# Performance work log

Hardware: AMD Instinct MI355X
Metric: run time of the kernel (lower is better)

## Reference

```python
import jax, jax.numpy as jnp
import numpy as np

D = 1024      # model_dim
H = 2048      # expert hidden_dim
E = 8         # num routed experts
S = 1         # num shared experts
M = 4         # num modes (1 shared expert per mode)
TOP_K = 2
B, L = 2, 2048


def _ffn(x, w1, b1, w2, b2):
    # x: [T, D]; w1: [..., D, H]; stacked experts via einsum
    h = jnp.einsum('td,edh->teh', x, w1) + b1          # [T, E*, H]
    h = jax.nn.gelu(h)
    return jnp.einsum('teh,ehd->ted', h, w2) + b2      # [T, E*, D]


def setup_inputs() -> dict:
    key = jax.random.key(0)
    ks = jax.random.split(key, 16)
    s = 0.02
    inp = {
        'hidden': jax.random.normal(ks[0], (B, L, D), dtype=jnp.float32),
        'mode_ids': jax.random.randint(ks[1], (B, L), 0, M),
        'router_w': jax.random.normal(ks[2], (D, E), dtype=jnp.float32) * s,
        'router_b': jnp.zeros((E,), dtype=jnp.float32),
        'shared_w1': jax.random.normal(ks[3], (S, D, H), dtype=jnp.float32) * s,
        'shared_b1': jnp.zeros((S, H), dtype=jnp.float32),
        'shared_w2': jax.random.normal(ks[4], (S, H, D), dtype=jnp.float32) * s,
        'shared_b2': jnp.zeros((S, D), dtype=jnp.float32),
        'mode_w1': jax.random.normal(ks[5], (M, D, H), dtype=jnp.float32) * s,
        'mode_b1': jnp.zeros((M, H), dtype=jnp.float32),
        'mode_w2': jax.random.normal(ks[6], (M, H, D), dtype=jnp.float32) * s,
        'mode_b2': jnp.zeros((M, D), dtype=jnp.float32),
        'routed_w1': jax.random.normal(ks[7], (E, D, H), dtype=jnp.float32) * s,
        'routed_b1': jnp.zeros((E, H), dtype=jnp.float32),
        'routed_w2': jax.random.normal(ks[8], (E, H, D), dtype=jnp.float32) * s,
        'routed_b2': jnp.zeros((E, D), dtype=jnp.float32),
    }
    return inp


def reference(hidden, mode_ids, router_w, router_b,
              shared_w1, shared_b1, shared_w2, shared_b2,
              mode_w1, mode_b1, mode_w2, mode_b2,
              routed_w1, routed_b1, routed_w2, routed_b2):
    b, l, d = hidden.shape
    flat = hidden.reshape(b * l, d)                         # [T, D]

    # --- router ---
    router_logits = flat @ router_w + router_b              # [T, E]
    router_probs = jax.nn.softmax(router_logits, axis=-1)
    topk_probs, topk_indices = jax.lax.top_k(router_probs, TOP_K)  # [T, K]

    # --- shared experts (mean over S experts) ---
    shared_out = _ffn(flat, shared_w1, shared_b1, shared_w2, shared_b2).mean(axis=1)  # [T, D]

    # --- mode-conditioned shared experts (1 expert per mode) ---
    mode_flat = mode_ids.reshape(-1)                        # [T]
    mode_onehot = jax.nn.one_hot(mode_flat, M, dtype=flat.dtype)   # [T, M]
    mode_all = _ffn(flat, mode_w1, mode_b1, mode_w2, mode_b2)      # [T, M, D]
    mode_out = jnp.einsum('tm,tmd->td', mode_onehot, mode_all)
    shared_out = shared_out + mode_out

    # --- routed experts: combine weights per (token, expert) ---
    # w[t,e] = sum_k topk_probs[t,k] * (topk_indices[t,k] == e)
    combine_w = jnp.einsum('tke,tk->te',
                           jax.nn.one_hot(topk_indices, E, dtype=flat.dtype),
                           topk_probs)                      # [T, E]
    routed_all = _ffn(flat, routed_w1, routed_b1, routed_w2, routed_b2)  # [T, E, D]
    mixed = jnp.einsum('te,ted->td', combine_w, routed_all)

    output = (shared_out + mixed).reshape(b, l, d)
    aux_logits = router_logits.reshape(b, l, E)
    aux_idx = topk_indices.reshape(b, l, TOP_K)
    aux_probs = topk_probs.reshape(b, l, TOP_K)
    return output, aux_logits, aux_idx, aux_probs
```

## Files before the change

kernel.cpp:

```cpp
#include <hip/hip_runtime.h>
#include <hip/hip_bf16.h>

typedef __hip_bfloat16 bf16t;
using f32x4 = __attribute__((ext_vector_type(4))) float;
using s16x8 = __attribute__((ext_vector_type(8))) short;

#define NTOK 4096
#define DIM 1024
#define HID 2048
#define NEXP 8
#define NMODE 4
#define NGRP 13
#define SLOTS_PAD 16640
#define MAXT 144

static constexpr size_t SZ_WT    = (size_t)NGRP * HID * DIM * 2;
static constexpr size_t OFF_WT1  = 0;
static constexpr size_t OFF_OBUF = 0;
static constexpr size_t OFF_WT2  = OFF_WT1 + SZ_WT;
static constexpr size_t OFF_HBUF = OFF_WT2 + SZ_WT;
static constexpr size_t SZ_HBUF  = (size_t)SLOTS_PAD * HID * 2;
static constexpr size_t OFF_XBF  = OFF_HBUF + SZ_HBUF;
static constexpr size_t SZ_XBF   = (size_t)NTOK * DIM * 2;
static constexpr size_t OFF_B1   = OFF_XBF + SZ_XBF;
static constexpr size_t OFF_B2   = OFF_B1 + (size_t)NGRP * HID * 4;
static constexpr size_t OFF_TP   = OFF_B2 + (size_t)NGRP * DIM * 4;
static constexpr size_t OFF_TI   = OFF_TP + (size_t)NTOK * 2 * 4;
static constexpr size_t OFF_MS   = OFF_TI + (size_t)NTOK * 2 * 4;
static constexpr size_t OFF_R0S  = OFF_MS + (size_t)NTOK * 4;
static constexpr size_t OFF_R1S  = OFF_R0S + (size_t)NTOK * 4;
static constexpr size_t OFF_LIST = OFF_R1S + (size_t)NTOK * 4;
static constexpr size_t OFF_CNT  = OFF_LIST + (size_t)SLOTS_PAD * 4;
static constexpr size_t OFF_CUR  = OFF_CNT + 64;
static constexpr size_t OFF_TC   = OFF_CUR + 64;
static constexpr size_t OFF_TD   = OFF_TC + 16;
static constexpr size_t WS_NEED  = OFF_TD + (size_t)MAXT * 16;

static __device__ __forceinline__ short fb(float f) {
    bf16t h = __float2bfloat16(f);
    short s; __builtin_memcpy(&s, &h, 2); return s;
}
static __device__ __forceinline__ float bf2f(short s) {
    unsigned u = ((unsigned)(unsigned short)s) << 16;
    float f; __builtin_memcpy(&f, &u, 4); return f;
}

static __device__ __forceinline__ float fast_exp(float x) {
#if __has_builtin(__builtin_amdgcn_exp2f)
    return __builtin_amdgcn_exp2f(x * 1.4426950408889634f);
#else
    return exp2f(x * 1.4426950408889634f);
#endif
}
static __device__ __forceinline__ float fast_rcp(float x) {
#if __has_builtin(__builtin_amdgcn_rcpf)
    return __builtin_amdgcn_rcpf(x);
#else
    return 1.0f / x;
#endif
}
static __device__ __forceinline__ float gelu_tanh(float x) {
    float x2 = x * x;
    float u = 0.7978845608028654f * fmaf(0.044715f * x2, x, x);
    u = fminf(u, 15.0f);
    float t = fast_exp(2.0f * u);
    return x * t * fast_rcp(t + 1.0f);
}

typedef __attribute__((address_space(3))) void lds_void;
typedef const __attribute__((address_space(1))) void gbl_void;
static __device__ __forceinline__ void gload16(const void* g, void* l) {
    __builtin_amdgcn_global_load_lds((gbl_void*)g, (lds_void*)l, 16, 0, 0);
}

#define TGRID1 3328
#define TGRID2 6656
#define RGRID  7680
#define PGRID  7784

struct TPtr {
    const float* s_w1; const float* s_w2;
    const float* m_w1; const float* m_w2;
    const float* r_w1; const float* r_w2;
};

__global__ __launch_bounds__(256) void prep_k(
    TPtr tp, bf16t* __restrict__ wt1, bf16t* __restrict__ wt2,
    const float* __restrict__ hidden, const int* __restrict__ mode_ids,
    const float* __restrict__ rw, const float* __restrict__ rb,
    float* __restrict__ aux_logits, float* __restrict__ aux_idx, float* __restrict__ aux_probs,
    float* __restrict__ topk_p, int* __restrict__ topk_i, bf16t* __restrict__ xbf,
    const float* __restrict__ sb1, const float* __restrict__ mb1, const float* __restrict__ rb1,
    const float* __restrict__ sb2, const float* __restrict__ mb2, const float* __restrict__ rb2,
    float* __restrict__ B1c, float* __restrict__ B2c) {
    const int bid = blockIdx.x;
    const int t = threadIdx.x;

    if (bid < TGRID2) {
        __shared__ float lds[2][64][65];
        const size_t MSZ = (size_t)DIM * HID;
        const float* src; bf16t* dst; int R, C, x, y;
        if (bid < TGRID1) {
            const int z = bid >> 8, rem = bid & 255;
            x = (rem >> 3) & 31; y = rem & 7;
            R = DIM; C = HID;
            if (z == 0)      { src = tp.s_w1;                       dst = wt1; }
            else if (z < 5)  { src = tp.m_w1 + (size_t)(z - 1) * MSZ; dst = wt1 + (size_t)z * MSZ; }
            else             { src = tp.r_w1 + (size_t)(z - 5) * MSZ; dst = wt1 + (size_t)z * MSZ; }
        } else {
            const int id2 = bid - TGRID1;
            const int z = id2 >> 8, rem = id2 & 255;
            x = rem >> 4; y = rem & 15;
            R = HID; C = DIM;
            if (z == 0)      { src = tp.s_w2;                       dst = wt2; }
            else if (z < 5)  { src = tp.m_w2 + (size_t)(z - 1) * MSZ; dst = wt2 + (size_t)z * MSZ; }
            else             { src = tp.r_w2 + (size_t)(z - 5) * MSZ; dst = wt2 + (size_t)z * MSZ; }
        }
        const int c0 = x * 64;
        const int ar = t >> 4, ac = (t & 15) * 4;
        const int bc = t >> 3;
        const int rg = (t & 7) * 8;
#pragma unroll
        for (int it = 0; it < 2; ++it) {
            const int r0 = (y * 2 + it) * 64;
#pragma unroll
            for (int p = 0; p < 4; p++) {
                const int r = p * 16 + ar;
                const float4 v = *(const float4*)(src + (size_t)(r0 + r) * C + (c0 + ac));
                lds[it][r][ac] = v.x; lds[it][r][ac + 1] = v.y;
                lds[it][r][ac + 2] = v.z; lds[it][r][ac + 3] = v.w;
            }
        }
        __syncthreads();
#pragma unroll
        for (int it = 0; it < 2; ++it) {
            const int r0 = (y * 2 + it) * 64;
#pragma unroll
            for (int j = 0; j < 2; j++) {
                const int c = j * 32 + bc;
                unsigned w[4];
#pragma unroll
                for (int u = 0; u < 4; u++) {
                    unsigned lo = (unsigned short)fb(lds[it][rg + 2 * u][c]);
                    unsigned hi = (unsigned short)fb(lds[it][rg + 2 * u + 1][c]);
                    w[u] = (hi << 16) | lo;
                }
                *(uint4*)((char*)dst + ((size_t)(c0 + c) * R + (r0 + rg)) * 2) = make_uint4(w[0], w[1], w[2], w[3]);
            }
        }
        return;
    }

    if (bid < RGRID) {
        const int tok = (bid - TGRID2) * 4 + (t >> 6);
        const int lane = t & 63;
        const float* x = hidden + (size_t)tok * DIM;
        float acc[NEXP];
#pragma unroll
        for (int e = 0; e < NEXP; e++) acc[e] = 0.f;
#pragma unroll
        for (int i = 0; i < DIM / 64; i++) {
            int d = i * 64 + lane;
            float xv = x[d];
            xbf[(size_t)tok * DIM + d] = __float2bfloat16(xv);
            const float4* w = (const float4*)(rw + (size_t)d * NEXP);
            float4 w0 = w[0], w1 = w[1];
            acc[0] += xv * w0.x; acc[1] += xv * w0.y; acc[2] += xv * w0.z; acc[3] += xv * w0.w;
            acc[4] += xv * w1.x; acc[5] += xv * w1.y; acc[6] += xv * w1.z; acc[7] += xv * w1.w;
        }
#pragma unroll
        for (int off = 32; off >= 1; off >>= 1) {
#pragma unroll
            for (int e = 0; e < NEXP; e++) acc[e] += __shfl_down(acc[e], off, 64);
        }
        if (lane == 0) {
            float lg[NEXP], pb[NEXP];
            float mx = -1e30f;
#pragma unroll
            for (int e = 0; e < NEXP; e++) { lg[e] = acc[e] + rb[e]; mx = fmaxf(mx, lg[e]); }
            float s = 0.f;
#pragma unroll
            for (int e = 0; e < NEXP; e++) { pb[e] = expf(lg[e] - mx); s += pb[e]; }
            float inv = 1.f / s;
#pragma unroll
            for (int e = 0; e < NEXP; e++) { pb[e] *= inv; aux_logits[(size_t)tok * NEXP + e] = lg[e]; }
            int i1 = 0;
            for (int e = 1; e < NEXP; e++) if (pb[e] > pb[i1]) i1 = e;
            int i2 = (i1 == 0) ? 1 : 0;
            for (int e = 0; e < NEXP; e++) { if (e == i1) continue; if (pb[e] > pb[i2]) i2 = e; }
            aux_idx[tok * 2] = (float)i1;  aux_idx[tok * 2 + 1] = (float)i2;
            aux_probs[tok * 2] = pb[i1];   aux_probs[tok * 2 + 1] = pb[i2];
            topk_p[tok * 2] = pb[i1];      topk_p[tok * 2 + 1] = pb[i2];
            topk_i[tok * 2] = i1;          topk_i[tok * 2 + 1] = i2;
        }
        return;
    }

    {
        const int i = (bid - RGRID) * 256 + t;
        if (i < NGRP * HID) {
            int g = i / HID, h = i % HID;
            B1c[i] = (g == 0) ? sb1[h] : (g < 5) ? mb1[(g - 1) * HID + h] : rb1[(g - 5) * HID + h];
        }
        if (i < NGRP * DIM) {
            int g = i / DIM, d = i % DIM;
            B2c[i] = (g == 0) ? sb2[d] : (g < 5) ? mb2[(g - 1) * DIM + d] : rb2[(g - 5) * DIM + d];
        }
    }
}

__global__ void count_k(const int* __restrict__ mode_ids, const int* __restrict__ topki,
                        int* __restrict__ cnts) {
    const int lane = threadIdx.x & 63;
    const int wave = threadIdx.x >> 6;
    int local[12];
#pragma unroll
    for (int i = 0; i < 12; i++) local[i] = 0;
    for (int c = blockIdx.x * 4 + wave; c < NTOK / 64; c += 32) {
        const int t = c * 64 + lane;
        const int m  = mode_ids[t];
        const int e0 = topki[t * 2];
        const int e1 = topki[t * 2 + 1];
#pragma unroll
        for (int b = 0; b < 4; b++) local[b] += __popcll(__ballot(m == b));
#pragma unroll
        for (int b = 0; b < 8; b++) {
            local[4 + b] += __popcll(__ballot(e0 == b));
            local[4 + b] += __popcll(__ballot(e1 == b));
        }
    }
    if (lane == 0) {
#pragma unroll
        for (int i = 0; i < 12; i++) atomicAdd(&cnts[i], local[i]);
    }
}

__global__ void scan_k(const int* __restrict__ cnts, int* __restrict__ cursors,
                       int4* __restrict__ tdesc, int* __restrict__ tcount) {
    if (threadIdx.x != 0 || blockIdx.x != 0) return;
    int nt = 0;
    auto emit = [&](int off, int c, int g) {
        for (int r0 = 0; r0 < c; r0 += 128) tdesc[nt++] = make_int4(off + r0, min(128, c - r0), g, 0);
    };
    emit(0, NTOK, 0);
    int off = NTOK;
    for (int m = 0; m < NMODE; m++) { cursors[m] = off; emit(off, cnts[m], 1 + m); off += cnts[m]; }
    off = 2 * NTOK;
    for (int e = 0; e < NEXP; e++) { cursors[NMODE + e] = off; emit(off, cnts[NMODE + e], 5 + e); off += cnts[NMODE + e]; }
    tcount[0] = nt;
}

__global__ void fill_k(const int* __restrict__ mode_ids, const int* __restrict__ topk_i,
                       int* __restrict__ cursors, int* __restrict__ list,
                       int* __restrict__ ms, int* __restrict__ r0s, int* __restrict__ r1s) {
    const int t = blockIdx.x * 256 + threadIdx.x;
    const int lane = threadIdx.x & 63;
    list[t] = t << 1;
    const int m  = mode_ids[t];
    const int e0 = topk_i[t * 2], e1 = topk_i[t * 2 + 1];

    auto put = [&](int bin, bool pred, int payload, int* inv) {
        unsigned long long msk = __ballot(pred);
        if (msk == 0ull) return;
        int leader = __ffsll((unsigned long long)msk) - 1;
        int base = 0;
        if (lane == leader) base = atomicAdd(&cursors[bin], __popcll(msk));
        base = __shfl(base, leader, 64);
        if (pred) {
            int pos = base + __popcll(msk & ((1ull << lane) - 1ull));
            list[pos] = payload;
            inv[t] = pos;
        }
    };
#pragma unroll
    for (int b = 0; b < NMODE; b++) put(b, m == b, t << 1, ms);
#pragma unroll
    for (int b = 0; b < NEXP; b++) put(NMODE + b, e0 == b, t << 1, r0s);
#pragma unroll
    for (int b = 0; b < NEXP; b++) put(NMODE + b, e1 == b, (t << 1) | 1, r1s);
}

template <int STAGE>
__global__ __launch_bounds__(256, 3) void ffn_gemm_k(
    const bf16t* __restrict__ xbf,
    const bf16t* __restrict__ hbuf,
    const bf16t* __restrict__ wt,
    const float* __restrict__ bias,
    bf16t* __restrict__ obuf,
    const int* __restrict__ list,
    const int4* __restrict__ tdesc,
    const int* __restrict__ tcount) {
    constexpr int K   = (STAGE == 1) ? DIM : HID;
    constexpr int N   = (STAGE == 1) ? HID : DIM;
    constexpr int NK  = K / 32;
    constexpr int NTN = N / 128;
    constexpr int NWG = NTN * MAXT;

    const int lin = blockIdx.x;
    const int wg  = (lin & 7) * (NWG >> 3) + (lin >> 3);
    const int ntile = wg / MAXT;
    const int tix = wg - ntile * MAXT;
    if (tix >= tcount[0]) return;
    const int4 td = tdesc[tix];
    const int slot0 = td.x, rows = td.y, gidx = td.z;
    const int n0 = ntile * 128;

    __shared__ alignas(16) char As[3 * 8192];
    __shared__ alignas(16) char Bs[3 * 8192];

    const int tid  = threadIdx.x;
    const int lane = tid & 63;
    const int w    = tid >> 6;
    const int wm   = w >> 1, wn = w & 1;

    const bf16t* wbase = wt + (size_t)gidx * ((size_t)K * N);
    const bf16t* aP[2];
    const bf16t* bP[2];
#pragma unroll
    for (int h = 0; h < 2; h++) {
        const int r  = (w * 2 + h) * 16 + (lane >> 2);
        const int ce = (((lane & 3) ^ ((r >> 1) & 3)) << 3);
        if (STAGE == 1) aP[h] = xbf + (size_t)(list[slot0 + r] >> 1) * DIM + ce;
        else            aP[h] = hbuf + (size_t)(slot0 + r) * HID + ce;
        bP[h] = wbase + (size_t)(n0 + r) * K + ce;
    }

    auto stage = [&](int t) {
        char* la = As + (t % 3) * 8192 + (w * 2) * 1024 + lane * 16;
        char* lb = Bs + (t % 3) * 8192 + (w * 2) * 1024 + lane * 16;
        gload16(aP[0] + t * 32, la);
        gload16(aP[1] + t * 32, la + 1024);
        gload16(bP[0] + t * 32, lb);
        gload16(bP[1] + t * 32, lb + 1024);
    };

    f32x4 acc[4][4];
    const f32x4 zero = {0.f, 0.f, 0.f, 0.f};
#pragma unroll
    for (int i = 0; i < 4; i++)
#pragma unroll
        for (int j = 0; j < 4; j++) acc[i][j] = zero;

    const int lm = lane & 15;
    const int kc = lane >> 4;

    stage(0); stage(1);

    for (int t = 0; t < NK; ++t) {
        const int cur = t % 3;
        if (t + 1 < NK) asm volatile("s_waitcnt vmcnt(4)" ::: "memory");
        else            asm volatile("s_waitcnt vmcnt(0)" ::: "memory");
        __builtin_amdgcn_s_barrier();

        s16x8 av[4], bv[4];
#pragma unroll
        for (int i = 0; i < 4; i++) {
            const int Ra = wm * 64 + i * 16 + lm;
            av[i] = *(const s16x8*)(As + cur * 8192 + Ra * 64 + ((kc ^ ((Ra >> 1) & 3)) << 4));
            const int Rb = wn * 64 + i * 16 + lm;
            bv[i] = *(const s16x8*)(Bs + cur * 8192 + Rb * 64 + ((kc ^ ((Rb >> 1) & 3)) << 4));
        }
        if (t + 2 < NK) stage(t + 2);

        __builtin_amdgcn_s_setprio(1);
#pragma unroll
        for (int mi = 0; mi < 4; mi++)
#pragma unroll
            for (int ni = 0; ni < 4; ni++)
                acc[mi][ni] = __builtin_amdgcn_mfma_f32_16x16x32_bf16(av[mi], bv[ni], acc[mi][ni], 0, 0, 0);
        __builtin_amdgcn_s_setprio(0);
    }

    const int lr = lane >> 4, lc = lane & 15;
#pragma unroll
    for (int ni = 0; ni < 4; ni++) {
        const int col = n0 + wn * 64 + ni * 16 + lc;
        const float bvv = bias[gidx * N + col];
#pragma unroll
        for (int mi = 0; mi < 4; mi++) {
#pragma unroll
            for (int r = 0; r < 4; r++) {
                const int row = wm * 64 + mi * 16 + lr * 4 + r;
                if (row < rows) {
                    float v = acc[mi][ni][r] + bvv;
                    if (STAGE == 1) v = gelu_tanh(v);
                    obuf[(size_t)(slot0 + row) * N + col] = __float2bfloat16(v);
                }
            }
        }
    }
}

__global__ void reduce_k(const bf16t* __restrict__ ob,
                         const int* __restrict__ ms, const int* __restrict__ r0s, const int* __restrict__ r1s,
                         const float* __restrict__ topkp, float* __restrict__ out) {
    const int t = blockIdx.x * 4 + (threadIdx.x >> 7);
    const int d = (threadIdx.x & 127) * 8;
    const s16x8 a = *(const s16x8*)(ob + (size_t)t * DIM + d);
    const s16x8 b = *(const s16x8*)(ob + (size_t)ms[t] * DIM + d);
    const s16x8 c = *(const s16x8*)(ob + (size_t)r0s[t] * DIM + d);
    const s16x8 e = *(const s16x8*)(ob + (size_t)r1s[t] * DIM + d);
    const float p0 = topkp[t * 2], p1 = topkp[t * 2 + 1];
    float o[8];
#pragma unroll
    for (int j = 0; j < 8; j++)
        o[j] = bf2f(a[j]) + bf2f(b[j]) + p0 * bf2f(c[j]) + p1 * bf2f(e[j]);
    float* dst = out + (size_t)t * DIM + d;
    *(float4*)dst = make_float4(o[0], o[1], o[2], o[3]);
    *(float4*)(dst + 4) = make_float4(o[4], o[5], o[6], o[7]);
}

extern "C" void kernel_launch(void* const* d_in, const int* in_sizes, int n_in,
                              void* d_out, int out_size, void* d_ws, size_t ws_size,
                              hipStream_t stream) {
    (void)in_sizes; (void)n_in; (void)out_size;
    if (ws_size < WS_NEED) return;

    const float* hidden   = (const float*)d_in[0];
    const int*   mode_ids = (const int*)d_in[1];
    const float* router_w = (const float*)d_in[2];
    const float* router_b = (const float*)d_in[3];
    TPtr tp;
    tp.s_w1 = (const float*)d_in[4];
    const float* s_b1 = (const float*)d_in[5];
    tp.s_w2 = (const float*)d_in[6];
    const float* s_b2 = (const float*)d_in[7];
    tp.m_w1 = (const float*)d_in[8];
    const float* m_b1 = (const float*)d_in[9];
    tp.m_w2 = (const float*)d_in[10];
    const float* m_b2 = (const float*)d_in[11];
    tp.r_w1 = (const float*)d_in[12];
    const float* r_b1 = (const float*)d_in[13];
    tp.r_w2 = (const float*)d_in[14];
    const float* r_b2 = (const float*)d_in[15];

    char* ws = (char*)d_ws;
    bf16t* WT1   = (bf16t*)(ws + OFF_WT1);
    bf16t* WT2   = (bf16t*)(ws + OFF_WT2);
    bf16t* Hbuf  = (bf16t*)(ws + OFF_HBUF);
    bf16t* Xbf   = (bf16t*)(ws + OFF_XBF);
    bf16t* Obuf  = (bf16t*)(ws + OFF_OBUF);
    float* B1c   = (float*)(ws + OFF_B1);
    float* B2c   = (float*)(ws + OFF_B2);
    float* topkp = (float*)(ws + OFF_TP);
    int*   topki = (int*)(ws + OFF_TI);
    int*   ms    = (int*)(ws + OFF_MS);
    int*   r0s   = (int*)(ws + OFF_R0S);
    int*   r1s   = (int*)(ws + OFF_R1S);
    int*   list  = (int*)(ws + OFF_LIST);
    int*   cnts  = (int*)(ws + OFF_CNT);
    int*   curs  = (int*)(ws + OFF_CUR);
    int*   tcnt  = (int*)(ws + OFF_TC);
    int4*  td    = (int4*)(ws + OFF_TD);

    float* out        = (float*)d_out;
    float* aux_logits = out + (size_t)NTOK * DIM;
    float* aux_idx    = aux_logits + (size_t)NTOK * NEXP;
    float* aux_probs  = aux_idx + (size_t)NTOK * 2;

    hipMemsetAsync(ws + OFF_LIST, 0, OFF_TC - OFF_LIST, stream);

    prep_k<<<PGRID, 256, 0, stream>>>(tp, WT1, WT2,
                                      hidden, mode_ids, router_w, router_b,
                                      aux_logits, aux_idx, aux_probs, topkp, topki, Xbf,
                                      s_b1, m_b1, r_b1, s_b2, m_b2, r_b2, B1c, B2c);
    count_k<<<8, 256, 0, stream>>>(mode_ids, topki, cnts);
    scan_k<<<1, 64, 0, stream>>>(cnts, curs, td, tcnt);
    fill_k<<<NTOK / 256, 256, 0, stream>>>(mode_ids, topki, curs, list, ms, r0s, r1s);
    ffn_gemm_k<1><<<(HID / 128) * MAXT, 256, 0, stream>>>(Xbf, Hbuf, WT1, B1c, Hbuf, list, td, tcnt);
    ffn_gemm_k<2><<<(DIM / 128) * MAXT, 256, 0, stream>>>(Xbf, Hbuf, WT2, B2c, Obuf, list, td, tcnt);
    reduce_k<<<NTOK / 4, 512, 0, stream>>>(Obuf, ms, r0s, r1s, topkp, out);
}
```

Baseline: 372.7 us.

## Move W2 weight transpose into stage-1 GEMM launch to overlap with compute

The fp32-to-bf16 transpose of the second-layer weights moves out of the prep kernel and into extra workgroups appended to the stage-1 GEMM grid. Those workgroups reuse the GEMM's shared-memory buffer, so the bandwidth-bound conversion can run alongside the compute-bound GEMM tiles instead of serially before routing. The prep kernel becomes smaller. The cost is that stage-1 GEMM blocks may compete for memory bandwidth and CUs with the transpose blocks, and early-exit GEMM tiles are interleaved with the transpose work.

```diff
diff --git a/kernel.cpp b/kernel.cpp
--- a/kernel.cpp
+++ b/kernel.cpp
@@ -73,19 +73,55 @@
     __builtin_amdgcn_global_load_lds((gbl_void*)g, (lds_void*)l, 16, 0, 0);
 }
 
-#define TGRID1 3328
-#define TGRID2 6656
-#define RGRID  7680
-#define PGRID  7784
-
 struct TPtr {
     const float* s_w1; const float* s_w2;
     const float* m_w1; const float* m_w2;
     const float* r_w1; const float* r_w2;
 };
 
+static __device__ __forceinline__ void transpose_tile(
+    const float* __restrict__ src, bf16t* __restrict__ dst, int R, int C, int x, int y,
+    float (*lds)[64][65], int t) {
+    const int c0 = x * 64;
+    const int ar = t >> 4, ac = (t & 15) * 4;
+    const int bc = t >> 3;
+    const int rg = (t & 7) * 8;
+#pragma unroll
+    for (int it = 0; it < 2; ++it) {
+        const int r0 = (y * 2 + it) * 64;
+#pragma unroll
+        for (int p = 0; p < 4; p++) {
+            const int r = p * 16 + ar;
+            const float4 v = *(const float4*)(src + (size_t)(r0 + r) * C + (c0 + ac));
+            lds[it][r][ac] = v.x; lds[it][r][ac + 1] = v.y;
+            lds[it][r][ac + 2] = v.z; lds[it][r][ac + 3] = v.w;
+        }
+    }
+    __syncthreads();
+#pragma unroll
+    for (int it = 0; it < 2; ++it) {
+        const int r0 = (y * 2 + it) * 64;
+#pragma unroll
+        for (int j = 0; j < 2; j++) {
+            const int c = j * 32 + bc;
+            unsigned w[4];
+#pragma unroll
+            for (int u = 0; u < 4; u++) {
+                unsigned lo = (unsigned short)fb(lds[it][rg + 2 * u][c]);
+                unsigned hi = (unsigned short)fb(lds[it][rg + 2 * u + 1][c]);
+                w[u] = (hi << 16) | lo;
+            }
+            *(uint4*)((char*)dst + ((size_t)(c0 + c) * R + (r0 + rg)) * 2) = make_uint4(w[0], w[1], w[2], w[3]);
+        }
+    }
+}
+
+#define TGRID1 3328
+#define RGRID  4352
+#define PGRID  4456
+
 __global__ __launch_bounds__(256) void prep_k(
-    TPtr tp, bf16t* __restrict__ wt1, bf16t* __restrict__ wt2,
+    TPtr tp, bf16t* __restrict__ wt1,
     const float* __restrict__ hidden, const int* __restrict__ mode_ids,
     const float* __restrict__ rw, const float* __restrict__ rb,
     float* __restrict__ aux_logits, float* __restrict__ aux_idx, float* __restrict__ aux_probs,
@@ -96,63 +132,21 @@
     const int bid = blockIdx.x;
     const int t = threadIdx.x;
 
-    if (bid < TGRID2) {
+    if (bid < TGRID1) {
         __shared__ float lds[2][64][65];
         const size_t MSZ = (size_t)DIM * HID;
-        const float* src; bf16t* dst; int R, C, x, y;
-        if (bid < TGRID1) {
-            const int z = bid >> 8, rem = bid & 255;
-            x = (rem >> 3) & 31; y = rem & 7;
-            R = DIM; C = HID;
-            if (z == 0)      { src = tp.s_w1;                       dst = wt1; }
-            else if (z < 5)  { src = tp.m_w1 + (size_t)(z - 1) * MSZ; dst = wt1 + (size_t)z * MSZ; }
-            else             { src = tp.r_w1 + (size_t)(z - 5) * MSZ; dst = wt1 + (size_t)z * MSZ; }
-        } else {
-            const int id2 = bid - TGRID1;
-            const int z = id2 >> 8, rem = id2 & 255;
-            x = rem >> 4; y = rem & 15;
-            R = HID; C = DIM;
-            if (z == 0)      { src = tp.s_w2;                       dst = wt2; }
-            else if (z < 5)  { src = tp.m_w2 + (size_t)(z - 1) * MSZ; dst = wt2 + (size_t)z * MSZ; }
-            else             { src = tp.r_w2 + (size_t)(z - 5) * MSZ; dst = wt2 + (size_t)z * MSZ; }
-        }
-        const int c0 = x * 64;
-        const int ar = t >> 4, ac = (t & 15) * 4;
-        const int bc = t >> 3;
-        const int rg = (t & 7) * 8;
-#pragma unroll
-        for (int it = 0; it < 2; ++it) {
-            const int r0 = (y * 2 + it) * 64;
-#pragma unroll
-            for (int p = 0; p < 4; p++) {
-                const int r = p * 16 + ar;
-                const float4 v = *(const float4*)(src + (size_t)(r0 + r) * C + (c0 + ac));
-                lds[it][r][ac] = v.x; lds[it][r][ac + 1] = v.y;
-                lds[it][r][ac + 2] = v.z; lds[it][r][ac + 3] = v.w;
-            }
-        }
-        __syncthreads();
-#pragma unroll
-        for (int it = 0; it < 2; ++it) {
-            const int r0 = (y * 2 + it) * 64;
-#pragma unroll
-            for (int j = 0; j < 2; j++) {
-                const int c = j * 32 + bc;
-                unsigned w[4];
-#pragma unroll
-                for (int u = 0; u < 4; u++) {
-                    unsigned lo = (unsigned short)fb(lds[it][rg + 2 * u][c]);
-                    unsigned hi = (unsigned short)fb(lds[it][rg + 2 * u + 1][c]);
-                    w[u] = (hi << 16) | lo;
-                }
-                *(uint4*)((char*)dst + ((size_t)(c0 + c) * R + (r0 + rg)) * 2) = make_uint4(w[0], w[1], w[2], w[3]);
-            }
-        }
+        const int z = bid >> 8, rem = bid & 255;
+        const int x = (rem >> 3) & 31, y = rem & 7;
+        const float* src;
+        if (z == 0)      src = tp.s_w1;
+        else if (z < 5)  src = tp.m_w1 + (size_t)(z - 1) * MSZ;
+        else             src = tp.r_w1 + (size_t)(z - 5) * MSZ;
+        transpose_tile(src, wt1 + (size_t)z * MSZ, DIM, HID, x, y, lds, t);
         return;
     }
 
     if (bid < RGRID) {
-        const int tok = (bid - TGRID2) * 4 + (t >> 6);
+        const int tok = (bid - TGRID1) * 4 + (t >> 6);
         const int lane = t & 63;
         const float* x = hidden + (size_t)tok * DIM;
         float acc[NEXP];
@@ -280,6 +274,7 @@
     for (int b = 0; b < NEXP; b++) put(NMODE + b, e1 == b, (t << 1) | 1, r1s);
 }
 
+#define W2GRID 3328
 template <int STAGE>
 __global__ __launch_bounds__(256, 3) void ffn_gemm_k(
     const bf16t* __restrict__ xbf,
@@ -289,12 +284,35 @@
     bf16t* __restrict__ obuf,
     const int* __restrict__ list,
     const int4* __restrict__ tdesc,
-    const int* __restrict__ tcount) {
+    const int* __restrict__ tcount,
+    const float* __restrict__ w2s, const float* __restrict__ w2m, const float* __restrict__ w2r,
+    bf16t* __restrict__ wt2o) {
     constexpr int K   = (STAGE == 1) ? DIM : HID;
     constexpr int N   = (STAGE == 1) ? HID : DIM;
     constexpr int NK  = K / 32;
     constexpr int NTN = N / 128;
     constexpr int NWG = NTN * MAXT;
+
+    __shared__ alignas(16) char smem[49152];
+
+    if constexpr (STAGE == 1) {
+        if (blockIdx.x >= NWG) {
+            const int id2 = blockIdx.x - NWG;
+            const size_t MSZ = (size_t)DIM * HID;
+            const int z = id2 >> 8, rem = id2 & 255;
+            const int x = rem >> 4, y = rem & 15;
+            const float* src;
+            if (z == 0)      src = w2s;
+            else if (z < 5)  src = w2m + (size_t)(z - 1) * MSZ;
+            else             src = w2r + (size_t)(z - 5) * MSZ;
+            transpose_tile(src, wt2o + (size_t)z * MSZ, HID, DIM, x, y,
+                           (float (*)[64][65])smem, threadIdx.x);
+            return;
+        }
+    }
+
+    char* As = smem;
+    char* Bs = smem + 24576;
 
     const int lin = blockIdx.x;
     const int wg  = (lin & 7) * (NWG >> 3) + (lin >> 3);
@@ -304,9 +322,6 @@
     const int4 td = tdesc[tix];
     const int slot0 = td.x, rows = td.y, gidx = td.z;
     const int n0 = ntile * 128;
-
-    __shared__ alignas(16) char As[3 * 8192];
-    __shared__ alignas(16) char Bs[3 * 8192];
 
     const int tid  = threadIdx.x;
     const int lane = tid & 63;
@@ -460,14 +475,16 @@
 
     hipMemsetAsync(ws + OFF_LIST, 0, OFF_TC - OFF_LIST, stream);
 
-    prep_k<<<PGRID, 256, 0, stream>>>(tp, WT1, WT2,
+    prep_k<<<PGRID, 256, 0, stream>>>(tp, WT1,
                                       hidden, mode_ids, router_w, router_b,
                                       aux_logits, aux_idx, aux_probs, topkp, topki, Xbf,
                                       s_b1, m_b1, r_b1, s_b2, m_b2, r_b2, B1c, B2c);
     count_k<<<8, 256, 0, stream>>>(mode_ids, topki, cnts);
     scan_k<<<1, 64, 0, stream>>>(cnts, curs, td, tcnt);
     fill_k<<<NTOK / 256, 256, 0, stream>>>(mode_ids, topki, curs, list, ms, r0s, r1s);
-    ffn_gemm_k<1><<<(HID / 128) * MAXT, 256, 0, stream>>>(Xbf, Hbuf, WT1, B1c, Hbuf, list, td, tcnt);
-    ffn_gemm_k<2><<<(DIM / 128) * MAXT, 256, 0, stream>>>(Xbf, Hbuf, WT2, B2c, Obuf, list, td, tcnt);
+    ffn_gemm_k<1><<<(HID / 128) * MAXT + W2GRID, 256, 0, stream>>>(
+        Xbf, Hbuf, WT1, B1c, Hbuf, list, td, tcnt, tp.s_w2, tp.m_w2, tp.r_w2, WT2);
+    ffn_gemm_k<2><<<(DIM / 128) * MAXT, 256, 0, stream>>>(
+        Xbf, Hbuf, WT2, B2c, Obuf, list, td, tcnt, nullptr, nullptr, nullptr, nullptr);
     reduce_k<<<NTOK / 4, 512, 0, stream>>>(Obuf, ms, r0s, r1s, topkp, out);
 }
```

New measurement: 346.9 us. 6.9% less time.
